# Kernel tuning notes

Measured on AMD Instinct MI355X. Metric: run time of the kernel, lower is better.

## Reference

```python
import jax, jax.numpy as jnp
import numpy as np


def _pairwise_sqdist(a, b):
    # a: [m, n, d], b: [m, n, d] -> M: [m, n, n], M[m,i,j] = ||a[m,i]-b[m,j]||^2
    # Use the expansion |a|^2 + |b|^2 - 2 a.b to avoid materializing the
    # [m, n, n, d] difference tensor; clamp tiny negatives from cancellation.
    a2 = jnp.sum(a * a, axis=-1)  # [m, n]
    b2 = jnp.sum(b * b, axis=-1)  # [m, n]
    ab = jnp.einsum('mid,mjd->mij', a, b)  # [m, n, n]
    return jnp.maximum(a2[:, :, None] + b2[:, None, :] - 2.0 * ab, 0.0)


def setup_inputs() -> dict:
    key = jax.random.key(0)
    k1, k2 = jax.random.split(key)
    template = jax.random.normal(k1, (16, 4096, 3), dtype=jnp.float32)
    source = jax.random.normal(k2, (16, 4096, 3), dtype=jnp.float32)
    return {"template": template, "source": source}


def reference(template, source):
    M = _pairwise_sqdist(template, source)  # [m, n, n]
    # min over template index (axis 1): nearest template point for each source point
    dist1 = jnp.mean(jnp.sqrt(jnp.min(M, axis=1)))
    # min over source index (axis 2): nearest source point for each template point
    dist2 = jnp.mean(jnp.sqrt(jnp.min(M, axis=2)))
    return (dist1 + dist2) / 2.0
```

## Files before the change

kernel.cpp:

```cpp
#include <hip/hip_runtime.h>

#define N_PTS   4096
#define N_BATCH 16
#define INV_CNT (1.0f / (2.0f * N_BATCH * N_PTS))
#define AROW_BYTES ((size_t)2 * N_BATCH * N_PTS * 16 * 2)
#define NBLK    512

typedef _Float16 f16x8  __attribute__((ext_vector_type(8)));
#define AS1 __attribute__((address_space(1)))
#define AS3 __attribute__((address_space(3)))

__global__ __launch_bounds__(256) void prep_kernel(
    const float* __restrict__ tpl, const float* __restrict__ src,
    _Float16* __restrict__ arow, float* __restrict__ out) {
    int pt = blockIdx.x * 256 + threadIdx.x;
    if (pt == 0) out[0] = 0.0f;
    const float* p = (pt < 65536 ? tpl : src) + (size_t)(pt & 65535) * 3;
    float x = p[0], y = p[1], z = p[2];
    float o2 = fmaf(x, x, fmaf(y, y, z * z));
    _Float16 xh = (_Float16)x, yh = (_Float16)y, zh = (_Float16)z;
    _Float16 xl = (_Float16)(x - (float)xh);
    _Float16 yl = (_Float16)(y - (float)yh);
    _Float16 zl = (_Float16)(z - (float)zh);
    _Float16 o2h = (_Float16)o2;
    _Float16 o2l = (_Float16)(o2 - (float)o2h);
    const _Float16 m2 = (_Float16)-2.0f;
    f16x8 v0, v1;
    v0[0] = m2 * xh; v0[1] = m2 * yh; v0[2] = m2 * zh;
    v0[3] = m2 * xl; v0[4] = m2 * yl; v0[5] = m2 * zl;
    v0[6] = m2 * xh; v0[7] = m2 * yh;
    v1[0] = m2 * zh; v1[1] = o2h; v1[2] = o2l;
    v1[3] = (_Float16)0.0f; v1[4] = (_Float16)0.0f; v1[5] = (_Float16)0.0f;
    v1[6] = (_Float16)0.0f; v1[7] = (_Float16)0.0f;
    *(f16x8*)(arow + (size_t)pt * 16)     = v0;
    *(f16x8*)(arow + (size_t)pt * 16 + 8) = v1;
}

#define FD(a,x,y) "v_min3_f32 %[" #a "], v" #x ", v" #y ", %[" #a "]\n\t"
#define FOLD_A FD(acc0,32,33) FD(acc1,34,35) FD(acc0,36,37) FD(acc1,38,39) \
               FD(acc0,40,41) FD(acc1,42,43) FD(acc0,44,45) FD(acc1,46,47) \
               FD(acc2,64,65) FD(acc3,66,67) FD(acc2,68,69) FD(acc3,70,71) \
               FD(acc2,72,73) FD(acc3,74,75) FD(acc2,76,77) FD(acc3,78,79)
#define FOLD_B FD(acc0,48,49) FD(acc1,50,51) FD(acc0,52,53) FD(acc1,54,55) \
               FD(acc0,56,57) FD(acc1,58,59) FD(acc0,60,61) FD(acc1,62,63) \
               FD(acc2,80,81) FD(acc3,82,83) FD(acc2,84,85) FD(acc3,86,87) \
               FD(acc2,88,89) FD(acc3,90,91) FD(acc2,92,93) FD(acc3,94,95)
#define MF_A(d) \
  "v_mfma_f32_32x32x16_f16 v[32:47], %[" #d "], %[bf0], v[96:111]\n\t" \
  "v_mfma_f32_32x32x16_f16 v[64:79], %[" #d "], %[bf1], v[96:111]\n\t"
#define MF_B(d) \
  "v_mfma_f32_32x32x16_f16 v[48:63], %[" #d "], %[bf0], v[96:111]\n\t" \
  "v_mfma_f32_32x32x16_f16 v[80:95], %[" #d "], %[bf1], v[96:111]\n\t"
#define DSR(d,off) "ds_read_b128 %[" #d "], %[dsa] offset:" #off "\n\t"
#define WL(n) "s_waitcnt lgkmcnt(" #n ")\n\t"
#define ZM(r) "v_mov_b32 v" #r ", 0\n\t"
#define NOP3 "s_nop 7\n\t" "s_nop 7\n\t" "s_nop 7\n\t"

__global__ __launch_bounds__(256, 2) void chamfer_mfma(
    const float* __restrict__ tpl, const float* __restrict__ src,
    const _Float16* __restrict__ arow, float* __restrict__ blocksum,
    float* __restrict__ out) {
    __shared__ uint4 sbuf[2][1024];
    __shared__ float wsum[4];

    const int tid = threadIdx.x;
    const int wv = tid >> 6, lane = tid & 63;
    const int n = lane & 31, g = lane >> 5;
    const int lin = blockIdx.x + 16 * (blockIdx.y + 16 * blockIdx.z);
    const int s_  = lin >> 3;
    const int qb  = s_ & 15;
    const int region = (lin & 7) + 8 * (s_ >> 4);
    const int batch  = region & 15;
    const int dir    = region >> 4;

    const float* qpts = (dir == 0) ? src : tpl;
    const _Float16* abase = arow + ((dir == 0) ? (size_t)0 : (size_t)65536 * 16)
                          + (size_t)batch * 4096 * 16;

    f16x8 bfr[2];
    float p2[2];
    #pragma unroll
    for (int i = 0; i < 2; ++i) {
        const int q = qb * 256 + wv * 64 + i * 32 + n;
        const float* p = qpts + (size_t)(batch * 4096 + q) * 3;
        float px = p[0], py = p[1], pz = p[2];
        p2[i] = fmaf(px, px, fmaf(py, py, pz * pz));
        _Float16 xh = (_Float16)px, yh = (_Float16)py, zh = (_Float16)pz;
        _Float16 xl = (_Float16)(px - (float)xh);
        _Float16 yl = (_Float16)(py - (float)yh);
        _Float16 zl = (_Float16)(pz - (float)zh);
        f16x8 b;
        if (g == 0) {
            b[0] = xh; b[1] = yh; b[2] = zh;
            b[3] = xh; b[4] = yh; b[5] = zh;
            b[6] = xl; b[7] = yl;
        } else {
            b[0] = zl; b[1] = (_Float16)1.0f; b[2] = (_Float16)1.0f;
            b[3] = (_Float16)0.0f; b[4] = (_Float16)0.0f; b[5] = (_Float16)0.0f;
            b[6] = (_Float16)0.0f; b[7] = (_Float16)0.0f;
        }
        bfr[i] = b;
    }

    const int lane_off = n * 32 + g * 16;
    const unsigned dsa0 = (unsigned)(size_t)((AS3 char*)&sbuf[0][0]) + lane_off;
    const unsigned dsa1 = (unsigned)(size_t)((AS3 char*)&sbuf[1][0]) + lane_off;

    const char* gwave = (const char*)abase + wv * 4096 + lane * 16;
    #define STAGE(ch)                                                          \
        {                                                                      \
            const char* gp = gwave + (size_t)(ch) * 16384;                     \
            AS3 char* lp = (AS3 char*)&sbuf[(ch) & 1][0] + wv * 4096;          \
            _Pragma("unroll")                                                  \
            for (int j = 0; j < 4; ++j)                                        \
                __builtin_amdgcn_global_load_lds(                              \
                    (const AS1 unsigned*)(gp + j * 1024),                      \
                    (AS3 unsigned*)(lp + j * 1024), 16, 0, 0);                 \
        }

    float acc0 = 1e30f, acc1 = 1e30f, acc2 = 1e30f, acc3 = 1e30f;
    f16x8 d0, d1, d2, d3;

    STAGE(0)
    #pragma unroll 1
    for (int c = 0; c < 8; ++c) {
        if (c < 7) STAGE(c + 1)
        if (c < 7)
            asm volatile("s_waitcnt vmcnt(4)\n\ts_barrier" ::: "memory");
        else
            asm volatile("s_waitcnt vmcnt(0)\n\ts_barrier" ::: "memory");
        const unsigned dsa = (c & 1) ? dsa1 : dsa0;

        asm volatile(
            ZM(96) ZM(97) ZM(98) ZM(99) ZM(100) ZM(101) ZM(102) ZM(103)
            ZM(104) ZM(105) ZM(106) ZM(107) ZM(108) ZM(109) ZM(110) ZM(111)
            DSR(d0,0) DSR(d1,1024) DSR(d2,2048) DSR(d3,3072)
            WL(3) MF_A(d0) DSR(d0,4096) NOP3
            WL(3) MF_B(d1) DSR(d1,5120)  FOLD_A
            WL(3) MF_A(d2) DSR(d2,6144)  FOLD_B
            WL(3) MF_B(d3) DSR(d3,7168)  FOLD_A
            WL(3) MF_A(d0) DSR(d0,8192)  FOLD_B
            WL(3) MF_B(d1) DSR(d1,9216)  FOLD_A
            WL(3) MF_A(d2) DSR(d2,10240) FOLD_B
            WL(3) MF_B(d3) DSR(d3,11264) FOLD_A
            WL(3) MF_A(d0) DSR(d0,12288) FOLD_B
            WL(3) MF_B(d1) DSR(d1,13312) FOLD_A
            WL(3) MF_A(d2) DSR(d2,14336) FOLD_B
            WL(3) MF_B(d3) DSR(d3,15360) FOLD_A
            WL(3) MF_A(d0) FOLD_B
            WL(2) MF_B(d1) FOLD_A
            WL(1) MF_A(d2) FOLD_B
            WL(0) MF_B(d3) FOLD_A
            NOP3 FOLD_B
            : [d0]"=&v"(d0), [d1]"=&v"(d1), [d2]"=&v"(d2), [d3]"=&v"(d3),
              [acc0]"+v"(acc0), [acc1]"+v"(acc1),
              [acc2]"+v"(acc2), [acc3]"+v"(acc3)
            : [bf0]"v"(bfr[0]), [bf1]"v"(bfr[1]), [dsa]"v"(dsa)
            : "memory",
              "v32","v33","v34","v35","v36","v37","v38","v39",
              "v40","v41","v42","v43","v44","v45","v46","v47",
              "v48","v49","v50","v51","v52","v53","v54","v55",
              "v56","v57","v58","v59","v60","v61","v62","v63",
              "v64","v65","v66","v67","v68","v69","v70","v71",
              "v72","v73","v74","v75","v76","v77","v78","v79",
              "v80","v81","v82","v83","v84","v85","v86","v87",
              "v88","v89","v90","v91","v92","v93","v94","v95",
              "v96","v97","v98","v99","v100","v101","v102","v103",
              "v104","v105","v106","v107","v108","v109","v110","v111");

        asm volatile("s_barrier" ::: "memory");
    }

    float v0 = fminf(acc0, acc1);
    v0 = fminf(v0, __shfl_xor(v0, 32));
    float v1 = fminf(acc2, acc3);
    v1 = fminf(v1, __shfl_xor(v1, 32));
    float dd0 = fmaxf(v0 + p2[0], 0.0f);
    float dd1 = fmaxf(v1 + p2[1], 0.0f);
    float s = (sqrtf(dd0) + sqrtf(dd1)) * INV_CNT;
    if (g != 0) s = 0.0f;
    #pragma unroll
    for (int off = 32; off > 0; off >>= 1) s += __shfl_down(s, off);
    if (lane == 0) wsum[wv] = s;
    __syncthreads();
    if (tid == 0) {
        float t = wsum[0] + wsum[1] + wsum[2] + wsum[3];
        if (blocksum) {
            int flat = (dir * N_BATCH + batch) * 16 + qb;
            blocksum[flat] = t;
        } else {
            atomicAdd(out, t);
        }
    }
}

__global__ __launch_bounds__(256) void final_kernel(
    const float* __restrict__ blocksum, float* __restrict__ out) {
    __shared__ float wsum[4];
    float s = 0.0f;
    #pragma unroll
    for (int j = 0; j < NBLK / 256; ++j)
        s += blocksum[j * 256 + threadIdx.x];
    #pragma unroll
    for (int off = 32; off > 0; off >>= 1) s += __shfl_down(s, off);
    if ((threadIdx.x & 63) == 0) wsum[threadIdx.x >> 6] = s;
    __syncthreads();
    if (threadIdx.x == 0) out[0] = wsum[0] + wsum[1] + wsum[2] + wsum[3];
}

extern "C" void kernel_launch(void* const* d_in, const int* in_sizes, int n_in,
                              void* d_out, int out_size, void* d_ws, size_t ws_size,
                              hipStream_t stream) {
    const float* tpl = (const float*)d_in[0];
    const float* src = (const float*)d_in[1];
    float* out = (float*)d_out;
    _Float16* arow = (_Float16*)d_ws;
    const bool roomy = ws_size >= AROW_BYTES + NBLK * sizeof(float);
    float* blocksum = roomy ? (float*)((char*)d_ws + AROW_BYTES) : nullptr;

    hipLaunchKernelGGL(prep_kernel, dim3((2 * N_BATCH * N_PTS) / 256),
                       dim3(256), 0, stream, tpl, src, arow, out);
    dim3 grid(N_PTS / 256, N_BATCH, 2);
    hipLaunchKernelGGL(chamfer_mfma, grid, dim3(256), 0, stream,
                       tpl, src, arow, blocksum, out);
    if (roomy)
        hipLaunchKernelGGL(final_kernel, dim3(1), dim3(256), 0, stream,
                           blocksum, out);
}
```

Baseline: 74.91 us.

## Split key range across wave pairs and double grid for higher occupancy

```diff
diff --git a/kernel.cpp b/kernel.cpp
--- a/kernel.cpp
+++ b/kernel.cpp
@@ -4,7 +4,7 @@
 #define N_BATCH 16
 #define INV_CNT (1.0f / (2.0f * N_BATCH * N_PTS))
 #define AROW_BYTES ((size_t)2 * N_BATCH * N_PTS * 16 * 2)
-#define NBLK    512
+#define NBLK    1024
 
 typedef _Float16 f16x8  __attribute__((ext_vector_type(8)));
 #define AS1 __attribute__((address_space(1)))
@@ -56,20 +56,22 @@
 #define ZM(r) "v_mov_b32 v" #r ", 0\n\t"
 #define NOP3 "s_nop 7\n\t" "s_nop 7\n\t" "s_nop 7\n\t"
 
-__global__ __launch_bounds__(256, 2) void chamfer_mfma(
+__global__ __launch_bounds__(256, 4) void chamfer_mfma(
     const float* __restrict__ tpl, const float* __restrict__ src,
     const _Float16* __restrict__ arow, float* __restrict__ blocksum,
     float* __restrict__ out) {
-    __shared__ uint4 sbuf[2][1024];
+    __shared__ uint4 sbuf[2][2][512];
+    __shared__ float cmb[2][2][2][32];
     __shared__ float wsum[4];
 
     const int tid = threadIdx.x;
     const int wv = tid >> 6, lane = tid & 63;
     const int n = lane & 31, g = lane >> 5;
-    const int lin = blockIdx.x + 16 * (blockIdx.y + 16 * blockIdx.z);
+    const int qg = wv & 1, kh = wv >> 1;
+    const int lin = blockIdx.x + 32 * (blockIdx.y + 16 * blockIdx.z);
     const int s_  = lin >> 3;
-    const int qb  = s_ & 15;
-    const int region = (lin & 7) + 8 * (s_ >> 4);
+    const int qb  = s_ & 31;
+    const int region = (lin & 7) + 8 * (s_ >> 5);
     const int batch  = region & 15;
     const int dir    = region >> 4;
 
@@ -81,7 +83,7 @@
     float p2[2];
     #pragma unroll
     for (int i = 0; i < 2; ++i) {
-        const int q = qb * 256 + wv * 64 + i * 32 + n;
+        const int q = qb * 128 + qg * 64 + i * 32 + n;
         const float* p = qpts + (size_t)(batch * 4096 + q) * 3;
         float px = p[0], py = p[1], pz = p[2];
         p2[i] = fmaf(px, px, fmaf(py, py, pz * pz));
@@ -102,21 +104,23 @@
         bfr[i] = b;
     }
 
-    const int lane_off = n * 32 + g * 16;
-    const unsigned dsa0 = (unsigned)(size_t)((AS3 char*)&sbuf[0][0]) + lane_off;
-    const unsigned dsa1 = (unsigned)(size_t)((AS3 char*)&sbuf[1][0]) + lane_off;
-
-    const char* gwave = (const char*)abase + wv * 4096 + lane * 16;
+    const char* gstage = (const char*)abase + (wv >> 1) * 65536
+                       + (wv & 1) * 1024 + lane * 16;
     #define STAGE(ch)                                                          \
         {                                                                      \
-            const char* gp = gwave + (size_t)(ch) * 16384;                     \
-            AS3 char* lp = (AS3 char*)&sbuf[(ch) & 1][0] + wv * 4096;          \
+            const char* gp = gstage + (ch) * 8192;                             \
+            AS3 char* lp = (AS3 char*)&sbuf[wv >> 1][(ch) & 1][0]              \
+                         + (wv & 1) * 1024;                                    \
             _Pragma("unroll")                                                  \
             for (int j = 0; j < 4; ++j)                                        \
                 __builtin_amdgcn_global_load_lds(                              \
-                    (const AS1 unsigned*)(gp + j * 1024),                      \
-                    (AS3 unsigned*)(lp + j * 1024), 16, 0, 0);                 \
-        }
+                    (const AS1 unsigned*)(gp + j * 2048),                      \
+                    (AS3 unsigned*)(lp + j * 2048), 16, 0, 0);                 \
+        }
+
+    const int lane_off = n * 32 + g * 16;
+    const unsigned dsa0 = (unsigned)(size_t)((AS3 char*)&sbuf[kh][0][0]) + lane_off;
+    const unsigned dsa1 = (unsigned)(size_t)((AS3 char*)&sbuf[kh][1][0]) + lane_off;
 
     float acc0 = 1e30f, acc1 = 1e30f, acc2 = 1e30f, acc3 = 1e30f;
     f16x8 d0, d1, d2, d3;
@@ -124,11 +128,12 @@
     STAGE(0)
     #pragma unroll 1
     for (int c = 0; c < 8; ++c) {
-        if (c < 7) STAGE(c + 1)
-        if (c < 7)
+        if (c < 7) {
+            STAGE(c + 1)
             asm volatile("s_waitcnt vmcnt(4)\n\ts_barrier" ::: "memory");
-        else
+        } else {
             asm volatile("s_waitcnt vmcnt(0)\n\ts_barrier" ::: "memory");
+        }
         const unsigned dsa = (c & 1) ? dsa1 : dsa0;
 
         asm volatile(
@@ -136,17 +141,9 @@
             ZM(104) ZM(105) ZM(106) ZM(107) ZM(108) ZM(109) ZM(110) ZM(111)
             DSR(d0,0) DSR(d1,1024) DSR(d2,2048) DSR(d3,3072)
             WL(3) MF_A(d0) DSR(d0,4096) NOP3
-            WL(3) MF_B(d1) DSR(d1,5120)  FOLD_A
-            WL(3) MF_A(d2) DSR(d2,6144)  FOLD_B
-            WL(3) MF_B(d3) DSR(d3,7168)  FOLD_A
-            WL(3) MF_A(d0) DSR(d0,8192)  FOLD_B
-            WL(3) MF_B(d1) DSR(d1,9216)  FOLD_A
-            WL(3) MF_A(d2) DSR(d2,10240) FOLD_B
-            WL(3) MF_B(d3) DSR(d3,11264) FOLD_A
-            WL(3) MF_A(d0) DSR(d0,12288) FOLD_B
-            WL(3) MF_B(d1) DSR(d1,13312) FOLD_A
-            WL(3) MF_A(d2) DSR(d2,14336) FOLD_B
-            WL(3) MF_B(d3) DSR(d3,15360) FOLD_A
+            WL(3) MF_B(d1) DSR(d1,5120) FOLD_A
+            WL(3) MF_A(d2) DSR(d2,6144) FOLD_B
+            WL(3) MF_B(d3) DSR(d3,7168) FOLD_A
             WL(3) MF_A(d0) FOLD_B
             WL(2) MF_B(d1) FOLD_A
             WL(1) MF_A(d2) FOLD_B
@@ -175,10 +172,20 @@
     v0 = fminf(v0, __shfl_xor(v0, 32));
     float v1 = fminf(acc2, acc3);
     v1 = fminf(v1, __shfl_xor(v1, 32));
-    float dd0 = fmaxf(v0 + p2[0], 0.0f);
-    float dd1 = fmaxf(v1 + p2[1], 0.0f);
-    float s = (sqrtf(dd0) + sqrtf(dd1)) * INV_CNT;
-    if (g != 0) s = 0.0f;
+    if (g == 0) {
+        cmb[qg][kh][0][n] = v0;
+        cmb[qg][kh][1][n] = v1;
+    }
+    __syncthreads();
+
+    float s = 0.0f;
+    if (kh == 0 && g == 0) {
+        float m0 = fminf(cmb[qg][0][0][n], cmb[qg][1][0][n]);
+        float m1 = fminf(cmb[qg][0][1][n], cmb[qg][1][1][n]);
+        float e0 = fmaxf(m0 + p2[0], 0.0f);
+        float e1 = fmaxf(m1 + p2[1], 0.0f);
+        s = (sqrtf(e0) + sqrtf(e1)) * INV_CNT;
+    }
     #pragma unroll
     for (int off = 32; off > 0; off >>= 1) s += __shfl_down(s, off);
     if (lane == 0) wsum[wv] = s;
@@ -186,7 +193,7 @@
     if (tid == 0) {
         float t = wsum[0] + wsum[1] + wsum[2] + wsum[3];
         if (blocksum) {
-            int flat = (dir * N_BATCH + batch) * 16 + qb;
+            int flat = (dir * N_BATCH + batch) * 32 + qb;
             blocksum[flat] = t;
         } else {
             atomicAdd(out, t);
@@ -220,7 +227,7 @@
 
     hipLaunchKernelGGL(prep_kernel, dim3((2 * N_BATCH * N_PTS) / 256),
                        dim3(256), 0, stream, tpl, src, arow, out);
-    dim3 grid(N_PTS / 256, N_BATCH, 2);
+    dim3 grid(32, N_BATCH, 2);
     hipLaunchKernelGGL(chamfer_mfma, grid, dim3(256), 0, stream,
                        tpl, src, arow, blocksum, out);
     if (roomy)
```

Result: slower. 77.81 us (+3.9%).
